# Kernel optimization log

Hardware: AMD Instinct MI355X
Metric: run time of the kernel (lower is better)

The kernel has to match this reference:

```python
import jax, jax.numpy as jnp
import numpy as np

KERNEL_MUL = 2.0
KERNEL_NUM = 5


def setup_inputs() -> dict:
    key = jax.random.key(0)
    k1, k2 = jax.random.split(key)
    source = jax.random.normal(k1, (4096, 256), dtype=jnp.float32)
    target = jax.random.normal(k2, (4096, 256), dtype=jnp.float32)
    return {"source": source, "target": target}


def reference(source, target):
    batch_size = source.shape[0]
    total = jnp.concatenate([source, target], axis=0)  # [2N, D]
    n_samples = total.shape[0]
    # avoids the [2N, 2N, D] expand the torch code materializes).
    sq = jnp.sum(total * total, axis=1)  # [2N]
    gram = total @ total.T               # [2N, 2N]
    L2 = sq[:, None] + sq[None, :] - 2.0 * gram
    # bandwidth computed from detached distances (torch uses .data)
    bw = jax.lax.stop_gradient(jnp.sum(L2)) / (n_samples ** 2 - n_samples)
    bw = bw / (KERNEL_MUL ** (KERNEL_NUM // 2))
    kernels = jnp.zeros_like(L2)
    for i in range(KERNEL_NUM):
        kernels = kernels + jnp.exp(-L2 / (bw * (KERNEL_MUL ** i)))
    XY = jnp.mean(kernels[:batch_size, batch_size:])
    YX = jnp.mean(kernels[batch_size:, :batch_size])
    loss = -XY - YX
    return loss
```

## Files before the change

kernel.cpp:

```cpp
#include <hip/hip_runtime.h>
#include <hip/hip_bf16.h>


#define D 256
#define NROWS 4096
#define SQ_OFF 4
#define S1PART 8196
#define CROSSPART 8452
#define COLPART 8708
#define ABF_OFF 74244
#define BBF_OFF 336388
#define WS_NEED_FLOATS 598532

typedef __attribute__((ext_vector_type(8))) short short8;
typedef __attribute__((ext_vector_type(16))) float float16;
typedef unsigned short ushort_t;

__device__ inline unsigned pack2_bf16(float a, float b) {
  unsigned ua = __float_as_uint(a);
  ua += 0x7FFFu + ((ua >> 16) & 1u);
  unsigned ub = __float_as_uint(b);
  ub += 0x7FFFu + ((ub >> 16) & 1u);
  return (ua >> 16) | (ub & 0xFFFF0000u);
}

__device__ inline void gload_lds16(const ushort_t* g, ushort_t* l) {
  __builtin_amdgcn_global_load_lds(
      (const __attribute__((address_space(1))) unsigned int*)g,
      (__attribute__((address_space(3))) unsigned int*)l, 16, 0, 0);
}

__global__ __launch_bounds__(256) void prep_kernel(const float* __restrict__ src,
                                                   const float* __restrict__ tgt,
                                                   float* __restrict__ ws,
                                                   int writeBf16) {
  __shared__ float csL[4][256];
  __shared__ float s1L[4];
  ushort_t* Abf = (ushort_t*)(ws + ABF_OFF);
  ushort_t* Bbf = (ushort_t*)(ws + BBF_OFF);
  int t = threadIdx.x;
  int wave = t >> 6, lane = t & 63;
  int rowBase = blockIdx.x * 32 + wave * 8;
  float cs0 = 0.f, cs1 = 0.f, cs2 = 0.f, cs3 = 0.f, s1 = 0.f;
#pragma unroll
  for (int r = 0; r < 8; ++r) {
    int row = rowBase + r;
    int isA = row < NROWS;
    const float* p = isA ? (src + (size_t)row * D) : (tgt + (size_t)(row - NROWS) * D);
    float4 v = reinterpret_cast<const float4*>(p)[lane];
    if (writeBf16) {
      ushort_t* dst = (isA ? Abf + (size_t)row * D : Bbf + (size_t)(row - NROWS) * D) + lane * 4;
      *reinterpret_cast<uint2*>(dst) = make_uint2(pack2_bf16(v.x, v.y), pack2_bf16(v.z, v.w));
    }
    cs0 += v.x; cs1 += v.y; cs2 += v.z; cs3 += v.w;
    float sq = v.x * v.x + v.y * v.y + v.z * v.z + v.w * v.w;
#pragma unroll
    for (int off = 32; off; off >>= 1) sq += __shfl_xor(sq, off, 64);
    if (lane == 0) { ws[SQ_OFF + row] = sq; s1 += sq; }
  }
  csL[wave][lane * 4 + 0] = cs0;
  csL[wave][lane * 4 + 1] = cs1;
  csL[wave][lane * 4 + 2] = cs2;
  csL[wave][lane * 4 + 3] = cs3;
  if (lane == 0) s1L[wave] = s1;
  __syncthreads();
  ws[COLPART + blockIdx.x * 256 + t] = csL[0][t] + csL[1][t] + csL[2][t] + csL[3][t];
  if (t == 0) ws[S1PART + blockIdx.x] = s1L[0] + s1L[1] + s1L[2] + s1L[3];
}

template <int BF16SRC>
__global__ __launch_bounds__(512, 2) void cross_kernel(const float* __restrict__ A32,
                                                       const float* __restrict__ B32,
                                                       const ushort_t* __restrict__ Abf,
                                                       const ushort_t* __restrict__ Bbf,
                                                       float* __restrict__ ws) {
  __shared__ ushort_t Ab[2][256 * 64];
  __shared__ ushort_t Bb[2][256 * 64];
  __shared__ float sqAs[256], sqBs[256];
  __shared__ float colhalf[2][256];
  __shared__ float redq[256];
  __shared__ float s1sh[256];
  __shared__ float red[8];
  __shared__ float c2sh;
  int t = threadIdx.x;
  int bid = blockIdx.x;

  int xcd = bid & 7, idx = bid >> 3;
  int bi = (xcd >> 1) * 4 + (idx >> 3);
  int bj = (xcd & 1) * 8 + (idx & 7);
  int rowBase = bi * 256, colBase = bj * 256;
  int wave = t >> 6, lane = t & 63;
  int wm = wave >> 2, wn = wave & 3;
  int hi = lane >> 5, lr = lane & 31;

  int grow = lane >> 3;
  int gchunk = (lane & 7) ^ grow;

  auto STAGE = [&](int buf, int k0) {
    if (BF16SRC) {
#pragma unroll
      for (int j = 0; j < 4; ++j) {
        int r0 = (wave * 4 + j) * 8;
        gload_lds16(Abf + (size_t)(rowBase + r0 + grow) * D + k0 + gchunk * 8, &Ab[buf][r0 * 64]);
        gload_lds16(Bbf + (size_t)(colBase + r0 + grow) * D + k0 + gchunk * 8, &Bb[buf][r0 * 64]);
      }
    } else {
#pragma unroll
      for (int i = 0; i < 4; ++i) {
        int r = (t >> 3) + 64 * i;
        int s = t & 7;
        int slot = (s ^ (r & 7)) << 3;
        const float* pa = &A32[(size_t)(rowBase + r) * D + k0 + s * 8];
        float4 a0 = *reinterpret_cast<const float4*>(pa);
        float4 a1 = *reinterpret_cast<const float4*>(pa + 4);
        *reinterpret_cast<uint4*>(&Ab[buf][r * 64 + slot]) =
            make_uint4(pack2_bf16(a0.x, a0.y), pack2_bf16(a0.z, a0.w),
                       pack2_bf16(a1.x, a1.y), pack2_bf16(a1.z, a1.w));
        const float* pb = &B32[(size_t)(colBase + r) * D + k0 + s * 8];
        float4 b0 = *reinterpret_cast<const float4*>(pb);
        float4 b1 = *reinterpret_cast<const float4*>(pb + 4);
        *reinterpret_cast<uint4*>(&Bb[buf][r * 64 + slot]) =
            make_uint4(pack2_bf16(b0.x, b0.y), pack2_bf16(b0.z, b0.w),
                       pack2_bf16(b1.x, b1.y), pack2_bf16(b1.z, b1.w));
      }
    }
  };

  STAGE(0, 0);

  {
    int col = t & 255, half = t >> 8;
    const float* cp = ws + COLPART + (size_t)half * 128 * 256 + col;
    float part = 0.f;
#pragma unroll 32
    for (int b = 0; b < 128; ++b) part += cp[(size_t)b * 256];
    colhalf[half][col] = part;
    if (t < 256) s1sh[t] = ws[S1PART + t];
  }
  __syncthreads();
  if (t < 256) { float c = colhalf[0][t] + colhalf[1][t]; redq[t] = c * c; }
  if (t < 256) sqAs[t] = ws[SQ_OFF + rowBase + t];
  else         sqBs[t - 256] = ws[SQ_OFF + NROWS + colBase + (t - 256)];
  __syncthreads();
  if (t < 64) {
    float r = redq[t] + redq[t + 64] + redq[t + 128] + redq[t + 192];
    float s = s1sh[t] + s1sh[t + 64] + s1sh[t + 128] + s1sh[t + 192];
#pragma unroll
    for (int off = 32; off; off >>= 1) {
      r += __shfl_xor(r, off, 64);
      s += __shfl_xor(s, off, 64);
    }
    if (t == 0) {
      double n = 8192.0;
      double sumL2 = 2.0 * n * (double)s - 2.0 * (double)r;
      double bwv = sumL2 / (n * n - n) / 4.0;
      c2sh = (float)(-1.4426950408889634 / (16.0 * bwv));
    }
  }

  float16 acc[4][2];
#pragma unroll
  for (int i = 0; i < 4; ++i)
#pragma unroll
    for (int j = 0; j < 2; ++j)
#pragma unroll
      for (int r = 0; r < 16; ++r) acc[i][j][r] = 0.f;

  auto COMPUTE = [&](int buf) {
#pragma unroll
    for (int ks = 0; ks < 4; ++ks) {
      int off = ((ks * 2 + hi) ^ (lr & 7)) << 3;
      short8 af[4], bf[2];
#pragma unroll
      for (int fr = 0; fr < 4; ++fr)
        af[fr] = *reinterpret_cast<const short8*>(&Ab[buf][(wm * 128 + fr * 32 + lr) * 64 + off]);
#pragma unroll
      for (int fc = 0; fc < 2; ++fc)
        bf[fc] = *reinterpret_cast<const short8*>(&Bb[buf][(wn * 64 + fc * 32 + lr) * 64 + off]);
      __builtin_amdgcn_s_setprio(1);
#pragma unroll
      for (int fr = 0; fr < 4; ++fr)
#pragma unroll
        for (int fc = 0; fc < 2; ++fc)
          acc[fr][fc] = __builtin_amdgcn_mfma_f32_32x32x16_bf16(af[fr], bf[fc], acc[fr][fc], 0, 0, 0);
      __builtin_amdgcn_s_setprio(0);
    }
  };

  __syncthreads();

  if (BF16SRC) {
#pragma unroll
    for (int step = 0; step < 4; ++step) {
      if (step < 3) STAGE((step + 1) & 1, (step + 1) * 64);
      if (step < 3) asm volatile("s_waitcnt vmcnt(8)" ::: "memory");
      else          asm volatile("s_waitcnt vmcnt(0)" ::: "memory");
      __builtin_amdgcn_s_barrier();
      COMPUTE(step & 1);
      if (step < 3) __builtin_amdgcn_s_barrier();
    }
  } else {
#pragma unroll
    for (int step = 0; step < 4; ++step) {
      if (step < 3) STAGE((step + 1) & 1, (step + 1) * 64);
      COMPUTE(step & 1);
      __syncthreads();
    }
  }

  float c2 = c2sh;
  float local = 0.f;
#pragma unroll
  for (int fr = 0; fr < 4; ++fr) {
#pragma unroll
    for (int fc = 0; fc < 2; ++fc) {
      float sB = sqBs[wn * 64 + fc * 32 + lr];
#pragma unroll
      for (int r = 0; r < 16; ++r) {
        int rrow = (r & 3) + 8 * (r >> 2) + 4 * hi;
        float dd = sqAs[wm * 128 + fr * 32 + rrow] + sB - 2.0f * acc[fr][fc][r];
        float y = __builtin_amdgcn_exp2f(dd * c2);
        float y2 = y * y, y4 = y2 * y2, y8 = y4 * y4, y16 = y8 * y8;
        local += y + y2 + y4 + y8 + y16;
      }
    }
  }
#pragma unroll
  for (int off = 32; off; off >>= 1) local += __shfl_xor(local, off, 64);
  if (lane == 0) red[wave] = local;
  __syncthreads();
  if (t == 0) {
    float s = 0.f;
#pragma unroll
    for (int i = 0; i < 8; ++i) s += red[i];
    ws[CROSSPART + bid] = s;
  }
}

__global__ __launch_bounds__(256) void finalize_kernel(const float* __restrict__ ws,
                                                       float* __restrict__ out) {
  __shared__ float red[256];
  int t = threadIdx.x;
  red[t] = ws[CROSSPART + t];
  __syncthreads();
#pragma unroll
  for (int s = 128; s > 0; s >>= 1) {
    if (t < s) red[t] += red[t + s];
    __syncthreads();
  }
  if (t == 0) out[0] = -2.0f * (red[0] * (1.0f / 16777216.0f));
}

extern "C" void kernel_launch(void* const* d_in, const int* in_sizes, int n_in,
                              void* d_out, int out_size, void* d_ws, size_t ws_size,
                              hipStream_t stream) {
  const float* src = (const float*)d_in[0];
  const float* tgt = (const float*)d_in[1];
  float* ws = (float*)d_ws;
  float* out = (float*)d_out;
  int useBf16 = ws_size >= (size_t)WS_NEED_FLOATS * sizeof(float);
  const ushort_t* Abf = (const ushort_t*)(ws + ABF_OFF);
  const ushort_t* Bbf = (const ushort_t*)(ws + BBF_OFF);

  prep_kernel<<<256, 256, 0, stream>>>(src, tgt, ws, useBf16);
  if (useBf16)
    cross_kernel<1><<<256, 512, 0, stream>>>(src, tgt, Abf, Bbf, ws);
  else
    cross_kernel<0><<<256, 512, 0, stream>>>(src, tgt, Abf, Bbf, ws);
  finalize_kernel<<<1, 256, 0, stream>>>(ws, out);
}
```

Baseline: 88.56 us.

## Compute bandwidth once in last prep block and fuse finalize into cross kernel

The column-sum and squared-norm reduction that sets the kernel bandwidth now runs once, in the last-arriving prep block, found with an atomic ticket counter. The result is stored to workspace, where cross blocks read one scalar instead of each block re-reducing the full 256x256 partial array. The separate finalize kernel is removed: the last cross block, again chosen by atomic ticket, sums the per-block partials and writes the output. This adds a memset to reset the counters, atomic and fence overhead, and a larger workspace requirement, since the B bf16 buffer offset moved and could trigger the fp32 fallback if the workspace is too small.

```diff
diff --git a/kernel.cpp b/kernel.cpp
--- a/kernel.cpp
+++ b/kernel.cpp
@@ -4,13 +4,14 @@
 
 #define D 256
 #define NROWS 4096
+#define C2S 2
 #define SQ_OFF 4
 #define S1PART 8196
 #define CROSSPART 8452
 #define COLPART 8708
 #define ABF_OFF 74244
-#define BBF_OFF 336388
-#define WS_NEED_FLOATS 598532
+#define BBF_OFF 598532
+#define WS_NEED_FLOATS 1122820
 
 typedef __attribute__((ext_vector_type(8))) short short8;
 typedef __attribute__((ext_vector_type(16))) float float16;
@@ -36,6 +37,7 @@
                                                    int writeBf16) {
   __shared__ float csL[4][256];
   __shared__ float s1L[4];
+  __shared__ int lastsh;
   ushort_t* Abf = (ushort_t*)(ws + ABF_OFF);
   ushort_t* Bbf = (ushort_t*)(ws + BBF_OFF);
   int t = threadIdx.x;
@@ -66,6 +68,38 @@
   __syncthreads();
   ws[COLPART + blockIdx.x * 256 + t] = csL[0][t] + csL[1][t] + csL[2][t] + csL[3][t];
   if (t == 0) ws[S1PART + blockIdx.x] = s1L[0] + s1L[1] + s1L[2] + s1L[3];
+
+  __threadfence();
+  __syncthreads();
+  if (t == 0) {
+    int ticket = __hip_atomic_fetch_add((int*)ws + 0, 1, __ATOMIC_ACQ_REL,
+                                        __HIP_MEMORY_SCOPE_AGENT);
+    lastsh = (ticket == (int)gridDim.x - 1);
+  }
+  __syncthreads();
+  if (lastsh) {
+    __builtin_amdgcn_fence(__ATOMIC_ACQUIRE, "agent");
+    float cs = 0.f;
+    const float* cp = ws + COLPART + t;
+#pragma unroll 32
+    for (int b = 0; b < 256; ++b) cs += cp[(size_t)b * 256];
+    float s1v = ws[S1PART + t];
+    __syncthreads();
+    csL[0][t] = cs * cs;
+    csL[1][t] = s1v;
+    __syncthreads();
+#pragma unroll
+    for (int s = 128; s > 0; s >>= 1) {
+      if (t < s) { csL[0][t] += csL[0][t + s]; csL[1][t] += csL[1][t + s]; }
+      __syncthreads();
+    }
+    if (t == 0) {
+      double n = 8192.0;
+      double sumL2 = 2.0 * n * (double)csL[1][0] - 2.0 * (double)csL[0][0];
+      double bwv = sumL2 / (n * n - n) / 4.0;
+      ws[C2S] = (float)(-1.4426950408889634 / (16.0 * bwv));
+    }
+  }
 }
 
 template <int BF16SRC>
@@ -73,15 +107,13 @@
                                                        const float* __restrict__ B32,
                                                        const ushort_t* __restrict__ Abf,
                                                        const ushort_t* __restrict__ Bbf,
-                                                       float* __restrict__ ws) {
+                                                       float* __restrict__ ws,
+                                                       float* __restrict__ out) {
   __shared__ ushort_t Ab[2][256 * 64];
   __shared__ ushort_t Bb[2][256 * 64];
   __shared__ float sqAs[256], sqBs[256];
-  __shared__ float colhalf[2][256];
-  __shared__ float redq[256];
-  __shared__ float s1sh[256];
   __shared__ float red[8];
-  __shared__ float c2sh;
+  __shared__ int lastsh;
   int t = threadIdx.x;
   int bid = blockIdx.x;
 
@@ -92,7 +124,6 @@
   int wave = t >> 6, lane = t & 63;
   int wm = wave >> 2, wn = wave & 3;
   int hi = lane >> 5, lr = lane & 31;
-
   int grow = lane >> 3;
   int gchunk = (lane & 7) ^ grow;
 
@@ -128,35 +159,9 @@
 
   STAGE(0, 0);
 
-  {
-    int col = t & 255, half = t >> 8;
-    const float* cp = ws + COLPART + (size_t)half * 128 * 256 + col;
-    float part = 0.f;
-#pragma unroll 32
-    for (int b = 0; b < 128; ++b) part += cp[(size_t)b * 256];
-    colhalf[half][col] = part;
-    if (t < 256) s1sh[t] = ws[S1PART + t];
-  }
-  __syncthreads();
-  if (t < 256) { float c = colhalf[0][t] + colhalf[1][t]; redq[t] = c * c; }
+  float c2 = ws[C2S];
   if (t < 256) sqAs[t] = ws[SQ_OFF + rowBase + t];
   else         sqBs[t - 256] = ws[SQ_OFF + NROWS + colBase + (t - 256)];
-  __syncthreads();
-  if (t < 64) {
-    float r = redq[t] + redq[t + 64] + redq[t + 128] + redq[t + 192];
-    float s = s1sh[t] + s1sh[t + 64] + s1sh[t + 128] + s1sh[t + 192];
-#pragma unroll
-    for (int off = 32; off; off >>= 1) {
-      r += __shfl_xor(r, off, 64);
-      s += __shfl_xor(s, off, 64);
-    }
-    if (t == 0) {
-      double n = 8192.0;
-      double sumL2 = 2.0 * n * (double)s - 2.0 * (double)r;
-      double bwv = sumL2 / (n * n - n) / 4.0;
-      c2sh = (float)(-1.4426950408889634 / (16.0 * bwv));
-    }
-  }
 
   float16 acc[4][2];
 #pragma unroll
@@ -208,7 +213,6 @@
     }
   }
 
-  float c2 = c2sh;
   float local = 0.f;
 #pragma unroll
   for (int fr = 0; fr < 4; ++fr) {
@@ -229,26 +233,32 @@
   for (int off = 32; off; off >>= 1) local += __shfl_xor(local, off, 64);
   if (lane == 0) red[wave] = local;
   __syncthreads();
+
   if (t == 0) {
     float s = 0.f;
 #pragma unroll
     for (int i = 0; i < 8; ++i) s += red[i];
     ws[CROSSPART + bid] = s;
-  }
-}
-
-__global__ __launch_bounds__(256) void finalize_kernel(const float* __restrict__ ws,
-                                                       float* __restrict__ out) {
-  __shared__ float red[256];
-  int t = threadIdx.x;
-  red[t] = ws[CROSSPART + t];
-  __syncthreads();
-#pragma unroll
-  for (int s = 128; s > 0; s >>= 1) {
-    if (t < s) red[t] += red[t + s];
+    __threadfence();
+    int ticket = __hip_atomic_fetch_add((int*)ws + 1, 1, __ATOMIC_ACQ_REL,
+                                        __HIP_MEMORY_SCOPE_AGENT);
+    lastsh = (ticket == (int)gridDim.x - 1);
+  }
+  __syncthreads();
+  if (lastsh) {
+    __builtin_amdgcn_fence(__ATOMIC_ACQUIRE, "agent");
+    float v = (t < 256) ? ws[CROSSPART + t] : 0.f;
+#pragma unroll
+    for (int off = 32; off; off >>= 1) v += __shfl_xor(v, off, 64);
+    if (lane == 0) red[wave] = v;
     __syncthreads();
-  }
-  if (t == 0) out[0] = -2.0f * (red[0] * (1.0f / 16777216.0f));
+    if (t == 0) {
+      float s = 0.f;
+#pragma unroll
+      for (int i = 0; i < 8; ++i) s += red[i];
+      out[0] = -2.0f * (s * (1.0f / 16777216.0f));
+    }
+  }
 }
 
 extern "C" void kernel_launch(void* const* d_in, const int* in_sizes, int n_in,
@@ -262,10 +272,10 @@
   const ushort_t* Abf = (const ushort_t*)(ws + ABF_OFF);
   const ushort_t* Bbf = (const ushort_t*)(ws + BBF_OFF);
 
+  hipMemsetAsync(d_ws, 0, 16, stream);
   prep_kernel<<<256, 256, 0, stream>>>(src, tgt, ws, useBf16);
   if (useBf16)
-    cross_kernel<1><<<256, 512, 0, stream>>>(src, tgt, Abf, Bbf, ws);
+    cross_kernel<1><<<256, 512, 0, stream>>>(src, tgt, Abf, Bbf, ws, out);
   else
-    cross_kernel<0><<<256, 512, 0, stream>>>(src, tgt, Abf, Bbf, ws);
-  finalize_kernel<<<1, 256, 0, stream>>>(ws, out);
-}
+    cross_kernel<0><<<256, 512, 0, stream>>>(src, tgt, Abf, Bbf, ws, out);
+}
```

Measured after the change: 122.2 us. 38.0% more time.
